# Performance work log

Hardware: AMD Instinct MI355X
Metric: run time of the kernel (lower is better)

## Reference

```python
import jax, jax.numpy as jnp
import numpy as np

N = 100000
E = 3200000
F_IN = 128
H1 = 16
H2 = 8
NEG_SLOPE = 0.2


def _gat_layer(x, src, dst, W, a_src, a_dst, b, n_nodes):
    # x: [N, Fin]; src/dst: [E_tot] (self-loops included); W: [Fin, Fout]
    h = x @ W                                   # [N, Fout]
    e_src = h @ a_src                           # [N]
    e_dst = h @ a_dst                           # [N]
    e = e_src[src] + e_dst[dst]                 # [E_tot]
    e = jnp.where(e > 0, e, NEG_SLOPE * e)      # leaky_relu(0.2)
    m = jax.ops.segment_max(e, dst, num_segments=n_nodes)   # [N]
    w = jnp.exp(e - m[dst])                     # [E_tot]
    s = jax.ops.segment_sum(w, dst, num_segments=n_nodes)   # [N]
    alpha = w / s[dst]                          # [E_tot]
    out = jax.ops.segment_sum(alpha[:, None] * h[src], dst, num_segments=n_nodes)
    return out + b


def setup_inputs() -> dict:
    key = jax.random.key(0)
    ks = jax.random.split(key, 12)
    x = jax.random.normal(ks[0], (N, F_IN), dtype=jnp.float32)
    edge_index = jax.random.randint(ks[1], (E, 2), 0, N, dtype=jnp.int64)
    s1 = 1.0 / np.sqrt(F_IN)
    s2 = 1.0 / np.sqrt(H1)
    s3 = 1.0 / np.sqrt(H2)
    return {
        "x": x,
        "edge_index": edge_index,
        "W1": jax.random.normal(ks[2], (F_IN, H1), dtype=jnp.float32) * s1,
        "a1_src": jax.random.normal(ks[3], (H1,), dtype=jnp.float32) * s2,
        "a1_dst": jax.random.normal(ks[4], (H1,), dtype=jnp.float32) * s2,
        "b1": jnp.zeros((H1,), dtype=jnp.float32),
        "W2": jax.random.normal(ks[5], (H1, H2), dtype=jnp.float32) * s2,
        "a2_src": jax.random.normal(ks[6], (H2,), dtype=jnp.float32) * s3,
        "a2_dst": jax.random.normal(ks[7], (H2,), dtype=jnp.float32) * s3,
        "b2": jnp.zeros((H2,), dtype=jnp.float32),
        "Wf": jax.random.normal(ks[8], (H2, 1), dtype=jnp.float32) * s3,
        "bf": jnp.zeros((1,), dtype=jnp.float32),
    }


def reference(x, edge_index, W1, a1_src, a1_dst, b1, W2, a2_src, a2_dst, b2, Wf, bf):
    ei = edge_index.T                            # [2, E] as in original forward
    loop = jnp.arange(N, dtype=ei.dtype)
    src = jnp.concatenate([ei[0], loop])         # PyG add_self_loops=True
    dst = jnp.concatenate([ei[1], loop])
    h = jax.nn.relu(_gat_layer(x, src, dst, W1, a1_src, a1_dst, b1, N))
    # dropout p=0.05 is identity at inference
    h = jax.nn.relu(_gat_layer(h, src, dst, W2, a2_src, a2_dst, b2, N))
    return h @ Wf + bf                           # [N, 1]
```

## Files before the change

### kernel.cpp

```cpp
#include <hip/hip_runtime.h>
#include <math.h>

#define N_NODES 100000
#define N_EDGES 3200000
#define E_TOT   (N_EDGES + N_NODES)
#define F_IN    128
#define H1      16
#define H2      8
#define NEG     0.2f
#define NBUCKET ((N_NODES + 255) >> 8)
#define NCHUNK  512
#define CE      ((N_EDGES + NCHUNK - 1) / NCHUNK)

typedef _Float16 half4v __attribute__((ext_vector_type(4)));

__global__ __launch_bounds__(256) void k1_xw(
        const float* __restrict__ x, const float* __restrict__ W1,
        const float* __restrict__ a1s, const float* __restrict__ a1d,
        _Float16* __restrict__ h1h, float* __restrict__ e1s, float* __restrict__ e1d) {
    __shared__ float w1s[F_IN * H1];
    __shared__ float xs[16 * 132];
    __shared__ float a1ss[H1], a1ds[H1];
    const int tid = threadIdx.x;
    for (int i = tid; i < F_IN * H1; i += 256) w1s[i] = W1[i];
    if (tid < H1) { a1ss[tid] = a1s[tid]; a1ds[tid] = a1d[tid]; }
    const int rowbase = blockIdx.x * 16;
    #pragma unroll
    for (int i = 0; i < 2; i++) {
        int q = tid + i * 256;
        int r = q >> 5, c = q & 31;
        float4 v = *(const float4*)(x + (size_t)(rowbase + r) * F_IN + c * 4);
        *(float4*)(xs + r * 132 + c * 4) = v;
    }
    __syncthreads();
    const int g = tid >> 4, j = tid & 15;
    const float* xrow = xs + g * 132;
    float acc = 0.f;
    #pragma unroll 8
    for (int k = 0; k < F_IN; k++) acc += xrow[k] * w1s[k * H1 + j];
    const int row = rowbase + g;
    h1h[(size_t)row * H1 + j] = (_Float16)acc;
    float ps = acc * a1ss[j];
    float pd = acc * a1ds[j];
    #pragma unroll
    for (int m = 8; m >= 1; m >>= 1) {
        ps += __shfl_xor(ps, m, 16);
        pd += __shfl_xor(pd, m, 16);
    }
    if (j == 0) { e1s[row] = ps; e1d[row] = pd; }
}


__global__ __launch_bounds__(256) void k_count(const int2* __restrict__ ei,
                                               int* __restrict__ counts) {
    __shared__ int hist[NBUCKET];
    for (int i = threadIdx.x; i < NBUCKET; i += 256) hist[i] = 0;
    __syncthreads();
    const int b = blockIdx.x;
    const int beg = b * CE, end = min(N_EDGES, beg + CE);
    for (int e = beg + threadIdx.x; e < end; e += 256)
        atomicAdd(&hist[ei[e].y >> 8], 1);
    __syncthreads();
    for (int i = threadIdx.x; i < NBUCKET; i += 256)
        counts[i * NCHUNK + b] = hist[i];
}

__global__ __launch_bounds__(512) void k_scanA(int* __restrict__ counts,
                                               int* __restrict__ btot) {
    __shared__ int lds[NCHUNK];
    const int k = blockIdx.x, t = threadIdx.x;
    int v = counts[k * NCHUNK + t];
    lds[t] = v;
    __syncthreads();
    for (int off = 1; off < NCHUNK; off <<= 1) {
        int u = (t >= off) ? lds[t - off] : 0;
        __syncthreads();
        lds[t] += u;
        __syncthreads();
    }
    counts[k * NCHUNK + t] = lds[t] - v;
    if (t == NCHUNK - 1) btot[k] = lds[t];
}

__global__ __launch_bounds__(512) void k_scanB(const int* __restrict__ btot,
                                               int* __restrict__ bbase) {
    __shared__ int lds[512];
    const int t = threadIdx.x;
    int v = (t < NBUCKET) ? btot[t] : 0;
    lds[t] = v;
    __syncthreads();
    for (int off = 1; off < 512; off <<= 1) {
        int u = (t >= off) ? lds[t - off] : 0;
        __syncthreads();
        lds[t] += u;
        __syncthreads();
    }
    if (t < NBUCKET) bbase[t] = lds[t] - v;
    if (t == 511) bbase[NBUCKET] = lds[511];
}

__global__ __launch_bounds__(256) void k_reorder(const int2* __restrict__ ei,
                                                 const int* __restrict__ counts,
                                                 const int* __restrict__ bbase,
                                                 int* __restrict__ pairs) {
    __shared__ int cur[NBUCKET];
    const int b = blockIdx.x;
    for (int i = threadIdx.x; i < NBUCKET; i += 256)
        cur[i] = bbase[i] + counts[i * NCHUNK + b];
    __syncthreads();
    const int beg = b * CE, end = min(N_EDGES, beg + CE);
    for (int e = beg + threadIdx.x; e < end; e += 256) {
        int2 v = ei[e];
        int k = v.y >> 8;
        int pos = atomicAdd(&cur[k], 1);
        pairs[pos] = (v.x << 8) | (v.y & 255);
    }
}

__global__ __launch_bounds__(256) void k_csr(const int* __restrict__ pairs,
                                             const int* __restrict__ bbase,
                                             int* __restrict__ rowg,
                                             int* __restrict__ degg,
                                             int* __restrict__ sorted_src) {
    __shared__ int deg[256], scn[256], cur[256];
    const int k = blockIdx.x, t = threadIdx.x;
    const int n0 = k << 8;
    const int nn = min(256, N_NODES - n0);
    deg[t] = 0;
    __syncthreads();
    const int ebeg = bbase[k], eend = bbase[k + 1];
    for (int e = ebeg + t; e < eend; e += 256)
        atomicAdd(&deg[pairs[e] & 255], 1);
    __syncthreads();
    int v = (t < nn) ? deg[t] : 0;
    scn[t] = v;
    __syncthreads();
    for (int off = 1; off < 256; off <<= 1) {
        int u = (t >= off) ? scn[t - off] : 0;
        __syncthreads();
        scn[t] += u;
        __syncthreads();
    }
    int excl = scn[t] - v;
    if (t < nn) {
        int r = ebeg + excl + n0 + t;
        rowg[n0 + t] = r;
        degg[n0 + t] = v + 1;
        sorted_src[r] = n0 + t;
        cur[t] = r + 1;
    }
    __syncthreads();
    for (int e = ebeg + t; e < eend; e += 256) {
        int p = pairs[e];
        int pos = atomicAdd(&cur[p & 255], 1);
        sorted_src[pos] = p >> 8;
    }
}

template <int LPN, int U, bool HALF, bool LAYER2>
__global__ __launch_bounds__(256) void k_agg(
        const int* __restrict__ row, const int* __restrict__ deg,
        const int* __restrict__ sorted_src,
        const float* __restrict__ es, const float* __restrict__ ed,
        const void* __restrict__ hbuf, const float* __restrict__ b,
        const float* __restrict__ Wf, const float* __restrict__ bf,
        float* __restrict__ h_out, float* __restrict__ out) {
    const int sub = threadIdx.x & (LPN - 1);
    const int node = (blockIdx.x * 256 + threadIdx.x) / LPN;
    if (node >= N_NODES) return;
    const int beg = row[node];
    const int cnt = deg[node];
    const float edv = ed[node];
    float4 acc = make_float4(0.f, 0.f, 0.f, 0.f);
    float s = 0.f;
    for (int t0 = 0; t0 < cnt; t0 += U) {
        int srcs[U];
        float evs[U];
        float4 hvs[U];
        #pragma unroll
        for (int i = 0; i < U; i++) {
            int idx = t0 + i;
            srcs[i] = sorted_src[beg + (idx < cnt ? idx : 0)];
        }
        #pragma unroll
        for (int i = 0; i < U; i++) {
            evs[i] = es[srcs[i]];
            if (HALF) {
                half4v hv = ((const half4v*)hbuf)[(size_t)srcs[i] * LPN + sub];
                hvs[i] = make_float4((float)hv.x, (float)hv.y, (float)hv.z, (float)hv.w);
            } else {
                hvs[i] = ((const float4*)hbuf)[(size_t)srcs[i] * LPN + sub];
            }
        }
        #pragma unroll
        for (int i = 0; i < U; i++) {
            if (t0 + i < cnt) {
                float e = evs[i] + edv;
                e = e > 0.f ? e : NEG * e;
                float p = __expf(e);
                s += p;
                acc.x += p * hvs[i].x;
                acc.y += p * hvs[i].y;
                acc.z += p * hvs[i].z;
                acc.w += p * hvs[i].w;
            }
        }
    }
    const float inv = 1.f / s;
    const float4 b4 = ((const float4*)b)[sub];
    float4 o;
    o.x = fmaxf(acc.x * inv + b4.x, 0.f);
    o.y = fmaxf(acc.y * inv + b4.y, 0.f);
    o.z = fmaxf(acc.z * inv + b4.z, 0.f);
    o.w = fmaxf(acc.w * inv + b4.w, 0.f);
    if (!LAYER2) {
        ((float4*)h_out)[(size_t)node * LPN + sub] = o;
    } else {
        const float4 w4 = ((const float4*)Wf)[sub];
        float r = o.x * w4.x + o.y * w4.y + o.z * w4.z + o.w * w4.w;
        r += __shfl_xor(r, 1, 2);
        if (sub == 0) out[node] = r + bf[0];
    }
}

__global__ __launch_bounds__(256) void k_mid(
        const float* __restrict__ h1f, const float* __restrict__ W2,
        const float* __restrict__ a2s, const float* __restrict__ a2d,
        float* __restrict__ h2, float* __restrict__ e2s, float* __restrict__ e2d) {
    int n = blockIdx.x * 256 + threadIdx.x;
    if (n >= N_NODES) return;
    float4 r0 = ((const float4*)(h1f + (size_t)n * H1))[0];
    float4 r1 = ((const float4*)(h1f + (size_t)n * H1))[1];
    float4 r2 = ((const float4*)(h1f + (size_t)n * H1))[2];
    float4 r3 = ((const float4*)(h1f + (size_t)n * H1))[3];
    float hv[H1] = {r0.x, r0.y, r0.z, r0.w, r1.x, r1.y, r1.z, r1.w,
                    r2.x, r2.y, r2.z, r2.w, r3.x, r3.y, r3.z, r3.w};
    float hs = 0.f, hd = 0.f;
    float* h2row = h2 + (size_t)n * H2;
    #pragma unroll
    for (int i = 0; i < H2; i++) {
        float acc = 0.f;
        #pragma unroll
        for (int j = 0; j < H1; j++) acc += hv[j] * W2[j * H2 + i];
        h2row[i] = acc;
        hs += acc * a2s[i];
        hd += acc * a2d[i];
    }
    e2s[n] = hs;
    e2d[n] = hd;
}

extern "C" void kernel_launch(void* const* d_in, const int* in_sizes, int n_in,
                              void* d_out, int out_size, void* d_ws, size_t ws_size,
                              hipStream_t stream) {
    const float* x    = (const float*)d_in[0];
    const int2*  ei   = (const int2*)d_in[1];
    const float* W1   = (const float*)d_in[2];
    const float* a1s  = (const float*)d_in[3];
    const float* a1d  = (const float*)d_in[4];
    const float* b1   = (const float*)d_in[5];
    const float* W2   = (const float*)d_in[6];
    const float* a2s  = (const float*)d_in[7];
    const float* a2d  = (const float*)d_in[8];
    const float* b2   = (const float*)d_in[9];
    const float* Wf   = (const float*)d_in[10];
    const float* bf   = (const float*)d_in[11];
    float* out = (float*)d_out;

    char* wp = (char*)d_ws;
    int* sorted_src = (int*)wp;   wp += sizeof(int) * (size_t)E_TOT;
    int* pairs      = (int*)wp;   wp += sizeof(int) * (size_t)N_EDGES;
    int* counts     = (int*)wp;   wp += sizeof(int) * (size_t)NBUCKET * NCHUNK;
    int* btot       = (int*)wp;   wp += sizeof(int) * (NBUCKET + 1);
    int* bbase      = (int*)wp;   wp += sizeof(int) * (NBUCKET + 1);
    int* degg       = (int*)wp;   wp += sizeof(int) * N_NODES;
    int* rowg       = (int*)wp;   wp += sizeof(int) * N_NODES;
    _Float16* h1h = (_Float16*)wp; wp += sizeof(_Float16) * (size_t)N_NODES * H1;
    float* e1s = (float*)wp;      wp += sizeof(float) * N_NODES;
    float* e1d = (float*)wp;      wp += sizeof(float) * N_NODES;
    float* h1f = (float*)pairs;
    float* h2  = h1f + (size_t)N_NODES * H1;
    float* e2s = h2 + (size_t)N_NODES * H2;
    float* e2d = e2s + N_NODES;

    const int nb_node = (N_NODES + 255) / 256;

    k_count<<<NCHUNK, 256, 0, stream>>>(ei, counts);
    k_scanA<<<NBUCKET, 512, 0, stream>>>(counts, btot);
    k_scanB<<<1, 512, 0, stream>>>(btot, bbase);
    k_reorder<<<NCHUNK, 256, 0, stream>>>(ei, counts, bbase, pairs);
    k_csr<<<NBUCKET, 256, 0, stream>>>(pairs, bbase, rowg, degg, sorted_src);
    k1_xw<<<N_NODES / 16, 256, 0, stream>>>(x, W1, a1s, a1d, h1h, e1s, e1d);
    k_agg<4, 8, true, false><<<(N_NODES * 4 + 255) / 256, 256, 0, stream>>>(
        rowg, degg, sorted_src, e1s, e1d, h1h, b1, nullptr, nullptr, h1f, nullptr);
    k_mid<<<nb_node, 256, 0, stream>>>(h1f, W2, a2s, a2d, h2, e2s, e2d);
    k_agg<2, 8, false, true><<<(N_NODES * 2 + 255) / 256, 256, 0, stream>>>(
        rowg, degg, sorted_src, e2s, e2d, h2, b2, Wf, bf, nullptr, out);
}
```

Measured before the change: 299.4 us.

## Fuse layer-2 projection into layer-1 aggregation and prefetch neighbor indices

```diff
diff --git a/kernel.cpp b/kernel.cpp
--- a/kernel.cpp
+++ b/kernel.cpp
@@ -11,6 +11,7 @@
 #define NBUCKET ((N_NODES + 255) >> 8)
 #define NCHUNK  512
 #define CE      ((N_EDGES + NCHUNK - 1) / NCHUNK)
+#define UA      8
 
 typedef _Float16 half4v __attribute__((ext_vector_type(4)));
 
@@ -59,7 +60,7 @@
     const int b = blockIdx.x;
     const int beg = b * CE, end = min(N_EDGES, beg + CE);
     for (int e = beg + threadIdx.x; e < end; e += 256)
-        atomicAdd(&hist[ei[e].y >> 8], 1);
+        atomicAdd(&hist[__builtin_nontemporal_load(&ei[e].y) >> 8], 1);
     __syncthreads();
     for (int i = threadIdx.x; i < NBUCKET; i += 256)
         counts[i * NCHUNK + b] = hist[i];
@@ -157,43 +158,48 @@
     }
 }
 
-template <int LPN, int U, bool HALF, bool LAYER2>
-__global__ __launch_bounds__(256) void k_agg(
+__global__ __launch_bounds__(256) void k_agg1(
         const int* __restrict__ row, const int* __restrict__ deg,
         const int* __restrict__ sorted_src,
         const float* __restrict__ es, const float* __restrict__ ed,
-        const void* __restrict__ hbuf, const float* __restrict__ b,
-        const float* __restrict__ Wf, const float* __restrict__ bf,
-        float* __restrict__ h_out, float* __restrict__ out) {
-    const int sub = threadIdx.x & (LPN - 1);
-    const int node = (blockIdx.x * 256 + threadIdx.x) / LPN;
+        const _Float16* __restrict__ h1h, const float* __restrict__ b1,
+        const float* __restrict__ W2, const float* __restrict__ a2s,
+        const float* __restrict__ a2d,
+        float* __restrict__ h2, float* __restrict__ e2s, float* __restrict__ e2d) {
+    __shared__ float w2s[H1 * H2];
+    __shared__ float a2ss[H2], a2ds[H2];
+    if (threadIdx.x < H1 * H2) w2s[threadIdx.x] = W2[threadIdx.x];
+    if (threadIdx.x < H2) { a2ss[threadIdx.x] = a2s[threadIdx.x]; a2ds[threadIdx.x] = a2d[threadIdx.x]; }
+    __syncthreads();
+    const int sub = threadIdx.x & 3;
+    const int node = (blockIdx.x * 256 + threadIdx.x) >> 2;
     if (node >= N_NODES) return;
     const int beg = row[node];
     const int cnt = deg[node];
+    const int last = beg + cnt - 1;
     const float edv = ed[node];
+    const half4v* h4 = (const half4v*)h1h;
     float4 acc = make_float4(0.f, 0.f, 0.f, 0.f);
     float s = 0.f;
-    for (int t0 = 0; t0 < cnt; t0 += U) {
-        int srcs[U];
-        float evs[U];
-        float4 hvs[U];
-        #pragma unroll
-        for (int i = 0; i < U; i++) {
-            int idx = t0 + i;
-            srcs[i] = sorted_src[beg + (idx < cnt ? idx : 0)];
+    int cur[UA], nxt[UA];
+    #pragma unroll
+    for (int i = 0; i < UA; i++)
+        cur[i] = __builtin_nontemporal_load(sorted_src + min(beg + i, last));
+    for (int t0 = 0; t0 < cnt; t0 += UA) {
+        float evs[UA];
+        float4 hvs[UA];
+        #pragma unroll
+        for (int i = 0; i < UA; i++) {
+            int sv = cur[i];
+            evs[i] = es[sv];
+            half4v hv = h4[(size_t)sv * 4 + sub];
+            hvs[i] = make_float4((float)hv.x, (float)hv.y, (float)hv.z, (float)hv.w);
         }
         #pragma unroll
-        for (int i = 0; i < U; i++) {
-            evs[i] = es[srcs[i]];
-            if (HALF) {
-                half4v hv = ((const half4v*)hbuf)[(size_t)srcs[i] * LPN + sub];
-                hvs[i] = make_float4((float)hv.x, (float)hv.y, (float)hv.z, (float)hv.w);
-            } else {
-                hvs[i] = ((const float4*)hbuf)[(size_t)srcs[i] * LPN + sub];
-            }
-        }
-        #pragma unroll
-        for (int i = 0; i < U; i++) {
+        for (int i = 0; i < UA; i++)
+            nxt[i] = __builtin_nontemporal_load(sorted_src + min(beg + t0 + UA + i, last));
+        #pragma unroll
+        for (int i = 0; i < UA; i++) {
             if (t0 + i < cnt) {
                 float e = evs[i] + edv;
                 e = e > 0.f ? e : NEG * e;
@@ -205,49 +211,96 @@
                 acc.w += p * hvs[i].w;
             }
         }
+        #pragma unroll
+        for (int i = 0; i < UA; i++) cur[i] = nxt[i];
     }
     const float inv = 1.f / s;
-    const float4 b4 = ((const float4*)b)[sub];
+    const float4 b4 = ((const float4*)b1)[sub];
     float4 o;
     o.x = fmaxf(acc.x * inv + b4.x, 0.f);
     o.y = fmaxf(acc.y * inv + b4.y, 0.f);
     o.z = fmaxf(acc.z * inv + b4.z, 0.f);
     o.w = fmaxf(acc.w * inv + b4.w, 0.f);
-    if (!LAYER2) {
-        ((float4*)h_out)[(size_t)node * LPN + sub] = o;
-    } else {
-        const float4 w4 = ((const float4*)Wf)[sub];
-        float r = o.x * w4.x + o.y * w4.y + o.z * w4.z + o.w * w4.w;
-        r += __shfl_xor(r, 1, 2);
-        if (sub == 0) out[node] = r + bf[0];
-    }
-}
-
-__global__ __launch_bounds__(256) void k_mid(
-        const float* __restrict__ h1f, const float* __restrict__ W2,
-        const float* __restrict__ a2s, const float* __restrict__ a2d,
-        float* __restrict__ h2, float* __restrict__ e2s, float* __restrict__ e2d) {
-    int n = blockIdx.x * 256 + threadIdx.x;
-    if (n >= N_NODES) return;
-    float4 r0 = ((const float4*)(h1f + (size_t)n * H1))[0];
-    float4 r1 = ((const float4*)(h1f + (size_t)n * H1))[1];
-    float4 r2 = ((const float4*)(h1f + (size_t)n * H1))[2];
-    float4 r3 = ((const float4*)(h1f + (size_t)n * H1))[3];
-    float hv[H1] = {r0.x, r0.y, r0.z, r0.w, r1.x, r1.y, r1.z, r1.w,
-                    r2.x, r2.y, r2.z, r2.w, r3.x, r3.y, r3.z, r3.w};
-    float hs = 0.f, hd = 0.f;
-    float* h2row = h2 + (size_t)n * H2;
+    float p2[H2];
+    const float* wr = w2s + (sub * 4) * H2;
+    #pragma unroll
+    for (int i = 0; i < H2; i++)
+        p2[i] = o.x * wr[i] + o.y * wr[H2 + i] + o.z * wr[2 * H2 + i] + o.w * wr[3 * H2 + i];
     #pragma unroll
     for (int i = 0; i < H2; i++) {
-        float acc = 0.f;
-        #pragma unroll
-        for (int j = 0; j < H1; j++) acc += hv[j] * W2[j * H2 + i];
-        h2row[i] = acc;
-        hs += acc * a2s[i];
-        hd += acc * a2d[i];
-    }
-    e2s[n] = hs;
-    e2d[n] = hd;
+        p2[i] += __shfl_xor(p2[i], 1, 4);
+        p2[i] += __shfl_xor(p2[i], 2, 4);
+    }
+    if (sub == 0) {
+        float hs = 0.f, hd = 0.f;
+        #pragma unroll
+        for (int i = 0; i < H2; i++) { hs += p2[i] * a2ss[i]; hd += p2[i] * a2ds[i]; }
+        e2s[node] = hs;
+        e2d[node] = hd;
+        ((float4*)h2)[(size_t)node * 2] = make_float4(p2[0], p2[1], p2[2], p2[3]);
+    } else if (sub == 1) {
+        ((float4*)h2)[(size_t)node * 2 + 1] = make_float4(p2[4], p2[5], p2[6], p2[7]);
+    }
+}
+
+__global__ __launch_bounds__(256) void k_agg2(
+        const int* __restrict__ row, const int* __restrict__ deg,
+        const int* __restrict__ sorted_src,
+        const float* __restrict__ es, const float* __restrict__ ed,
+        const float* __restrict__ h2, const float* __restrict__ b2,
+        const float* __restrict__ Wf, const float* __restrict__ bf,
+        float* __restrict__ out) {
+    const int sub = threadIdx.x & 1;
+    const int node = (blockIdx.x * 256 + threadIdx.x) >> 1;
+    if (node >= N_NODES) return;
+    const int beg = row[node];
+    const int cnt = deg[node];
+    const int last = beg + cnt - 1;
+    const float edv = ed[node];
+    const float4* h4 = (const float4*)h2;
+    float4 acc = make_float4(0.f, 0.f, 0.f, 0.f);
+    float s = 0.f;
+    int cur[UA], nxt[UA];
+    #pragma unroll
+    for (int i = 0; i < UA; i++)
+        cur[i] = __builtin_nontemporal_load(sorted_src + min(beg + i, last));
+    for (int t0 = 0; t0 < cnt; t0 += UA) {
+        float evs[UA];
+        float4 hvs[UA];
+        #pragma unroll
+        for (int i = 0; i < UA; i++) {
+            int sv = cur[i];
+            evs[i] = es[sv];
+            hvs[i] = h4[(size_t)sv * 2 + sub];
+        }
+        #pragma unroll
+        for (int i = 0; i < UA; i++)
+            nxt[i] = __builtin_nontemporal_load(sorted_src + min(beg + t0 + UA + i, last));
+        #pragma unroll
+        for (int i = 0; i < UA; i++) {
+            if (t0 + i < cnt) {
+                float e = evs[i] + edv;
+                e = e > 0.f ? e : NEG * e;
+                float p = __expf(e);
+                s += p;
+                acc.x += p * hvs[i].x;
+                acc.y += p * hvs[i].y;
+                acc.z += p * hvs[i].z;
+                acc.w += p * hvs[i].w;
+            }
+        }
+        #pragma unroll
+        for (int i = 0; i < UA; i++) cur[i] = nxt[i];
+    }
+    const float inv = 1.f / s;
+    const float4 b4 = ((const float4*)b2)[sub];
+    const float4 w4 = ((const float4*)Wf)[sub];
+    float r = fmaxf(acc.x * inv + b4.x, 0.f) * w4.x
+            + fmaxf(acc.y * inv + b4.y, 0.f) * w4.y
+            + fmaxf(acc.z * inv + b4.z, 0.f) * w4.z
+            + fmaxf(acc.w * inv + b4.w, 0.f) * w4.w;
+    r += __shfl_xor(r, 1, 2);
+    if (sub == 0) out[node] = r + bf[0];
 }
 
 extern "C" void kernel_launch(void* const* d_in, const int* in_sizes, int n_in,
@@ -278,12 +331,9 @@
     _Float16* h1h = (_Float16*)wp; wp += sizeof(_Float16) * (size_t)N_NODES * H1;
     float* e1s = (float*)wp;      wp += sizeof(float) * N_NODES;
     float* e1d = (float*)wp;      wp += sizeof(float) * N_NODES;
-    float* h1f = (float*)pairs;
-    float* h2  = h1f + (size_t)N_NODES * H1;
+    float* h2  = (float*)pairs;
     float* e2s = h2 + (size_t)N_NODES * H2;
     float* e2d = e2s + N_NODES;
-
-    const int nb_node = (N_NODES + 255) / 256;
 
     k_count<<<NCHUNK, 256, 0, stream>>>(ei, counts);
     k_scanA<<<NBUCKET, 512, 0, stream>>>(counts, btot);
@@ -291,9 +341,8 @@
     k_reorder<<<NCHUNK, 256, 0, stream>>>(ei, counts, bbase, pairs);
     k_csr<<<NBUCKET, 256, 0, stream>>>(pairs, bbase, rowg, degg, sorted_src);
     k1_xw<<<N_NODES / 16, 256, 0, stream>>>(x, W1, a1s, a1d, h1h, e1s, e1d);
-    k_agg<4, 8, true, false><<<(N_NODES * 4 + 255) / 256, 256, 0, stream>>>(
-        rowg, degg, sorted_src, e1s, e1d, h1h, b1, nullptr, nullptr, h1f, nullptr);
-    k_mid<<<nb_node, 256, 0, stream>>>(h1f, W2, a2s, a2d, h2, e2s, e2d);
-    k_agg<2, 8, false, true><<<(N_NODES * 2 + 255) / 256, 256, 0, stream>>>(
-        rowg, degg, sorted_src, e2s, e2d, h2, b2, Wf, bf, nullptr, out);
-}
+    k_agg1<<<(N_NODES * 4 + 255) / 256, 256, 0, stream>>>(
+        rowg, degg, sorted_src, e1s, e1d, h1h, b1, W2, a2s, a2d, h2, e2s, e2d);
+    k_agg2<<<(N_NODES * 2 + 255) / 256, 256, 0, stream>>>(
+        rowg, degg, sorted_src, e2s, e2d, h2, b2, Wf, bf, out);
+}
```

After: 381.0 us. 1.27x slower.
